# Performance work log

Hardware: AMD Instinct MI355X
Metric: run time of the kernel (lower is better)

Reference implementation:

```python
import jax, jax.numpy as jnp
import numpy as np

B, N, DIM = 2, 2048, 1024
H, DH = 16, 64            # num query heads, head dim (single shared kv head)
CTX_N, CTX_DIM = 256, 1024

def setup_inputs() -> dict:
    key = jax.random.key(0)
    ks = jax.random.split(key, 8)
    s = lambda fan: 1.0 / np.sqrt(fan)
    return {
        'x': jax.random.normal(ks[0], (B, N, DIM), jnp.float32),
        'context': jax.random.normal(ks[1], (B, CTX_N, CTX_DIM), jnp.float32),
        'g1': jnp.ones((DIM,), jnp.float32),
        'Wq': jax.random.normal(ks[2], (DIM, H * DH), jnp.float32) * s(DIM),
        'Wkv': jax.random.normal(ks[3], (DIM, 2 * DH), jnp.float32) * s(DIM),
        'null_kv': jax.random.normal(ks[4], (2, DH), jnp.float32) * s(DH),
        'ctx_g': jnp.ones((CTX_DIM,), jnp.float32),
        'ctx_b': jnp.zeros((CTX_DIM,), jnp.float32),
        'Wc': jax.random.normal(ks[5], (CTX_DIM, 2 * DH), jnp.float32) * s(CTX_DIM),
        'bc': jnp.zeros((2 * DH,), jnp.float32),
        'Wout': jax.random.normal(ks[6], (H * DH, DIM), jnp.float32) * s(H * DH),
        'g2': jnp.ones((DIM,), jnp.float32),
    }

def _ln_g(t, g, eps):
    # custom LayerNorm: scale only, no bias, population variance
    m = jnp.mean(t, axis=-1, keepdims=True)
    v = jnp.var(t, axis=-1, keepdims=True)
    return (t - m) / jnp.sqrt(v + eps) * g

def reference(x, context, g1, Wq, Wkv, null_kv, ctx_g, ctx_b, Wc, bc, Wout, g2):
    b, n, _ = x.shape
    scale = DH ** -0.5
    h = _ln_g(x, g1, 1e-5)                              # [b,n,dim]
    q = (h @ Wq).reshape(b, n, H, DH).transpose(0, 2, 1, 3) * scale  # [b,H,n,d]
    k, v = jnp.split(h @ Wkv, 2, axis=-1)               # each [b,n,d] (single kv head)
    # null kv token
    nk = jnp.broadcast_to(null_kv[0], (b, 1, DH))
    nv = jnp.broadcast_to(null_kv[1], (b, 1, DH))
    k = jnp.concatenate((k, nk), axis=-2)
    v = jnp.concatenate((v, nv), axis=-2)
    # context kv tokens (standard flax LayerNorm: scale+bias, eps=1e-6)
    cm = jnp.mean(context, axis=-1, keepdims=True)
    cv_ = jnp.var(context, axis=-1, keepdims=True)
    ch = (context - cm) / jnp.sqrt(cv_ + 1e-6) * ctx_g + ctx_b
    ck, cvv = jnp.split(ch @ Wc + bc, 2, axis=-1)       # [b,ctx_n,d]
    k = jnp.concatenate((k, ck), axis=-2)               # [b,j,d]
    v = jnp.concatenate((v, cvv), axis=-2)
    sim = jnp.einsum('bhid,bjd->bhij', q, k)            # shared kv head broadcast
    attn = jax.nn.softmax(sim, axis=-1)
    out = jnp.einsum('bhij,bjd->bhid', attn, v)
    out = out.transpose(0, 2, 1, 3).reshape(b, n, H * DH)
    out = out @ Wout
    return _ln_g(out, g2, 1e-5)
```

## Files before the change

### kernel.cpp

```cpp
#include <hip/hip_runtime.h>

typedef __attribute__((ext_vector_type(4)))  float  f32x4;
typedef __attribute__((ext_vector_type(16))) float  f32x16;
typedef __attribute__((ext_vector_type(8)))  short  s16x8;

#define DEVI __device__ __forceinline__

constexpr int Bb   = 2;
constexpr int Nn   = 2048;
constexpr int Hh   = 16;
constexpr int DHc  = 64;
constexpr int CTXN = 256;
constexpr int Jv   = Nn + 1 + CTXN;
constexpr int JP   = 2432;
constexpr int QKVN = Hh*DHc + 2*DHc;

DEVI unsigned short f2bf(float f) {
    union { float f; unsigned u; } v; v.f = f;
    unsigned r = v.u + 0x7fffu + ((v.u >> 16) & 1u);
    return (unsigned short)(r >> 16);
}
DEVI float bf2f(unsigned short h) {
    union { unsigned u; float f; } v; v.u = ((unsigned)h) << 16;
    return v.f;
}
DEVI unsigned cvt_pk_bf(float lo, float hi) {
    unsigned r;
    asm("v_cvt_pk_bf16_f32 %0, %1, %2" : "=v"(r) : "v"(lo), "v"(hi));
    return r;
}
DEVI float exp2v(float x) {
    float r;
    asm("v_exp_f32 %0, %1" : "=v"(r) : "v"(x));
    return r;
}
DEVI void gl_lds16(const void* g, void* l) {
    __builtin_amdgcn_global_load_lds(
        (__attribute__((address_space(1))) void*)g,
        (__attribute__((address_space(3))) void*)l,
        16, 0, 0);
}

__global__ __launch_bounds__(256) void k_pre(const float* __restrict__ Wq,
                                             const float* __restrict__ Wkv,
                                             const float* __restrict__ Wc,
                                             const float* __restrict__ Wout,
                                             const float* __restrict__ x,
                                             const float* __restrict__ ctx,
                                             const float* __restrict__ g1,
                                             const float* __restrict__ cg,
                                             const float* __restrict__ cb,
                                             unsigned short* __restrict__ WqkvT,
                                             unsigned short* __restrict__ WcT,
                                             unsigned short* __restrict__ WoutT,
                                             unsigned short* __restrict__ h,
                                             unsigned short* __restrict__ ch,
                                             float qscale) {
    int bxg = blockIdx.x;
    if (bxg < 2304) {
        __shared__ float tile[32][33];
        int bx = bxg % 72, by = bxg / 72;
        const float* in; unsigned short* out; int C; float scale; int cb_;
        if (bx < 32)      { in = Wq;   out = WqkvT;               C = 1024; scale = qscale; cb_ = bx; }
        else if (bx < 36) { in = Wkv;  out = WqkvT + 1024 * 1024; C = 128;  scale = 1.0f;  cb_ = bx - 32; }
        else if (bx < 40) { in = Wc;   out = WcT;                 C = 128;  scale = 1.0f;  cb_ = bx - 36; }
        else              { in = Wout; out = WoutT;               C = 1024; scale = 1.0f;  cb_ = bx - 40; }
        int tx = threadIdx.x & 31, ty = threadIdx.x >> 5;
        int r0 = by * 32, c0 = cb_ * 32;
#pragma unroll
        for (int i = 0; i < 32; i += 8)
            tile[ty + i][tx] = in[(size_t)(r0 + ty + i) * C + c0 + tx];
        __syncthreads();
#pragma unroll
        for (int i = 0; i < 32; i += 8)
            out[(size_t)(c0 + ty + i) * 1024 + r0 + tx] = f2bf(tile[tx][ty + i] * scale);
    } else {
        int row = bxg - 2304, tid = threadIdx.x;
        bool isx = row < 4096;
        const float* rp = isx ? x + (size_t)row * 1024 : ctx + (size_t)(row - 4096) * 1024;
        const float* g  = isx ? g1 : cg;
        float eps = isx ? 1e-5f : 1e-6f;
        unsigned short* o = isx ? h + (size_t)row * 1024 : ch + (size_t)(row - 4096) * 1024;

        f32x4 v = *(const f32x4*)(rp + tid * 4);
        float s = v.x + v.y + v.z + v.w;
        float q = v.x * v.x + v.y * v.y + v.z * v.z + v.w * v.w;
#pragma unroll
        for (int m = 32; m; m >>= 1) { s += __shfl_down(s, m, 64); q += __shfl_down(q, m, 64); }
        __shared__ float ss[4], sq[4];
        int wid = tid >> 6, lane = tid & 63;
        if (lane == 0) { ss[wid] = s; sq[wid] = q; }
        __syncthreads();
        s = ss[0] + ss[1] + ss[2] + ss[3];
        q = sq[0] + sq[1] + sq[2] + sq[3];
        float mean = s * (1.0f / 1024.0f);
        float var  = q * (1.0f / 1024.0f) - mean * mean;
        float rstd = rsqrtf(var + eps);
        f32x4 gg = *(const f32x4*)(g + tid * 4);
        f32x4 r;
#pragma unroll
        for (int e = 0; e < 4; e++) r[e] = (v[e] - mean) * rstd * gg[e];
        if (!isx) {
            f32x4 bb = *(const f32x4*)(cb + tid * 4);
#pragma unroll
            for (int e = 0; e < 4; e++) r[e] += bb[e];
        }
        uint2 ov = make_uint2(cvt_pk_bf(r[0], r[1]), cvt_pk_bf(r[2], r[3]));
        *(uint2*)(o + tid * 4) = ov;
    }
}

__global__ __launch_bounds__(256) void k_ln_out(const float* __restrict__ in,
                                                const float* __restrict__ g,
                                                float* __restrict__ out) {
    int row = blockIdx.x, tid = threadIdx.x;
    const float* rp = in + (size_t)row * 1024;
    f32x4 v = *(const f32x4*)(rp + tid * 4);
    float s = v.x + v.y + v.z + v.w;
    float q = v.x * v.x + v.y * v.y + v.z * v.z + v.w * v.w;
#pragma unroll
    for (int m = 32; m; m >>= 1) { s += __shfl_down(s, m, 64); q += __shfl_down(q, m, 64); }
    __shared__ float ss[4], sq[4];
    int wid = tid >> 6, lane = tid & 63;
    if (lane == 0) { ss[wid] = s; sq[wid] = q; }
    __syncthreads();
    s = ss[0] + ss[1] + ss[2] + ss[3];
    q = sq[0] + sq[1] + sq[2] + sq[3];
    float mean = s * (1.0f / 1024.0f);
    float var  = q * (1.0f / 1024.0f) - mean * mean;
    float rstd = rsqrtf(var + 1e-5f);
    f32x4 gg = *(const f32x4*)(g + tid * 4);
    f32x4 r;
#pragma unroll
    for (int e = 0; e < 4; e++) r[e] = (v[e] - mean) * rstd * gg[e];
    *(f32x4*)(out + (size_t)row * 1024 + tid * 4) = r;
}

template<int OUT_BF16>
__global__ __launch_bounds__(256) void k_gemm_bt(const unsigned short* __restrict__ A,
                                                 const unsigned short* __restrict__ BT,
                                                 void* __restrict__ C,
                                                 int M, int N, int K) {
    __shared__ unsigned short SA[2][128 * 64];
    __shared__ unsigned short SB[2][64 * 64];
    int tid = threadIdx.x;
    int bn = blockIdx.x, bm = blockIdx.y;
    int wid = tid >> 6, lane = tid & 63;
    int wm = wid >> 1, wn = wid & 1;
    int lr = lane & 15, lg = lane >> 4;
    int r8 = lane >> 3;
    int sl = (lane & 7) ^ r8;

    const unsigned short* Ag = A  + (size_t)(bm * 128 + wid * 32 + r8) * K + sl * 8;
    const unsigned short* Bg = BT + (size_t)(bn * 64  + wid * 16 + r8) * K + sl * 8;

    auto stage = [&](int k0, int buf) {
#pragma unroll
        for (int i = 0; i < 4; i++)
            gl_lds16(Ag + (size_t)i * 8 * K + k0, &SA[buf][wid * 2048 + i * 512]);
#pragma unroll
        for (int i = 0; i < 2; i++)
            gl_lds16(Bg + (size_t)i * 8 * K + k0, &SB[buf][wid * 1024 + i * 512]);
    };

    f32x4 acc[4][2] = {};
    int nk = K >> 6;
    stage(0, 0);
    __syncthreads();
    int cur = 0;
    for (int s = 0; s < nk; ++s) {
        if (s + 1 < nk) stage((s + 1) << 6, cur ^ 1);
        const unsigned short* Al = &SA[cur][0];
        const unsigned short* Bl = &SB[cur][0];
#pragma unroll
        for (int kk = 0; kk < 2; kk++) {
            int co = ((kk * 4 + lg) ^ (lr & 7)) * 8;
            s16x8 af[4], bf[2];
#pragma unroll
            for (int mi = 0; mi < 4; mi++)
                af[mi] = *(const s16x8*)&Al[(wm * 64 + mi * 16 + lr) * 64 + co];
#pragma unroll
            for (int ni = 0; ni < 2; ni++)
                bf[ni] = *(const s16x8*)&Bl[(wn * 32 + ni * 16 + lr) * 64 + co];
#pragma unroll
            for (int mi = 0; mi < 4; mi++)
#pragma unroll
                for (int ni = 0; ni < 2; ni++)
                    acc[mi][ni] = __builtin_amdgcn_mfma_f32_16x16x32_bf16(af[mi], bf[ni], acc[mi][ni], 0, 0, 0);
        }
        __syncthreads();
        cur ^= 1;
    }
#pragma unroll
    for (int mi = 0; mi < 4; mi++)
#pragma unroll
        for (int r = 0; r < 4; r++) {
            int row = bm * 128 + wm * 64 + mi * 16 + lg * 4 + r;
#pragma unroll
            for (int ni = 0; ni < 2; ni++) {
                int col = bn * 64 + wn * 32 + ni * 16 + lr;
                float val = acc[mi][ni][r];
                if (OUT_BF16)
                    ((unsigned short*)C)[(size_t)row * N + col] = f2bf(val);
                else
                    ((float*)C)[(size_t)row * N + col] = val;
            }
        }
}

__global__ __launch_bounds__(256) void k_assemble_kv(const unsigned short* __restrict__ qkv,
                                                     const unsigned short* __restrict__ ckv,
                                                     const float* __restrict__ nkv,
                                                     const float* __restrict__ bc,
                                                     unsigned short* __restrict__ Kb,
                                                     unsigned short* __restrict__ Vt) {
    int idx = blockIdx.x * 256 + threadIdx.x;
    int d = idx & 63;
    int j = (idx >> 6) % JP;
    int b = idx / (64 * JP);
    float kv, vv;
    if (j < Nn) {
        const unsigned short* r = qkv + (size_t)(b * Nn + j) * QKVN + Hh * DHc;
        kv = bf2f(r[d]); vv = bf2f(r[64 + d]);
    } else if (j == Nn) {
        kv = nkv[d]; vv = nkv[64 + d];
    } else if (j < Jv) {
        const unsigned short* r = ckv + (size_t)(b * CTXN + (j - Nn - 1)) * 128;
        kv = bf2f(r[d]) + bc[d]; vv = bf2f(r[64 + d]) + bc[64 + d];
    } else {
        kv = 0.0f; vv = 0.0f;
    }
    Kb[((size_t)b * JP + j) * 64 + d] = f2bf(kv);
    Vt[((size_t)b * 64 + d) * JP + j] = f2bf(vv);
}

__global__ __launch_bounds__(512) void k_attn(const unsigned short* __restrict__ qkv,
                                              const unsigned short* __restrict__ Kb,
                                              const unsigned short* __restrict__ Vt,
                                              unsigned short* __restrict__ aout) {
    __shared__ unsigned short KV[2][2][2][64 * 64];

    int bid = blockIdx.x;
    int qt = bid & 15, h = (bid >> 4) & 15, b = bid >> 8;
    int tid = threadIdx.x, wid = tid >> 6, lane = tid & 63;
    int tm = wid >> 2, tw = wid & 3;
    int l31 = lane & 31, hi = lane >> 5;
    int n0 = qt * 128 + tw * 32;
    int r8 = lane >> 3;
    int sl = (lane & 7) ^ r8;
    int x7 = l31 & 7;
    int jb = tm * 1216;

    s16x8 qf[4];
#pragma unroll
    for (int kk = 0; kk < 4; kk++)
        qf[kk] = *(const s16x8*)(qkv + (size_t)(b * Nn + n0 + l31) * QKVN + h * 64 + kk * 16 + hi * 8);

    f32x16 O0 = {}, O1 = {};
    float Lv = 0.0f;

    const unsigned short* Kg = Kb + ((size_t)b * JP + jb + tw * 16 + r8) * 64 + sl * 8;
    const unsigned short* Vg = Vt + ((size_t)b * 64 + tw * 16 + r8) * JP + jb + sl * 8;

    auto stage = [&](int t, int buf) {
#pragma unroll
        for (int i = 0; i < 2; i++) {
            gl_lds16(Kg + ((size_t)t * 64 + i * 8) * 64, &KV[tm][buf][0][tw * 1024 + i * 512]);
            gl_lds16(Vg + (size_t)i * 8 * JP + t * 64,   &KV[tm][buf][1][tw * 1024 + i * 512]);
        }
    };

    auto build_pf = [&](const f32x16& s, int w) -> s16x8 {
        unsigned c0 = cvt_pk_bf(s[8 * w + 0], s[8 * w + 1]);
        unsigned c1 = cvt_pk_bf(s[8 * w + 2], s[8 * w + 3]);
        unsigned c2 = cvt_pk_bf(s[8 * w + 4], s[8 * w + 5]);
        unsigned c3 = cvt_pk_bf(s[8 * w + 6], s[8 * w + 7]);
        asm("v_permlane32_swap_b32 %0, %1" : "+v"(c0), "+v"(c2));
        asm("v_permlane32_swap_b32 %0, %1" : "+v"(c1), "+v"(c3));
        union { unsigned u[4]; s16x8 v; } pu;
        pu.u[0] = c0; pu.u[1] = c1; pu.u[2] = c2; pu.u[3] = c3;
        return pu.v;
    };

    stage(0, 0);
    __syncthreads();
    int cur = 0;
#pragma unroll 1
    for (int t = 0; t < 19; ++t) {
        if (t < 18) stage(t + 1, cur ^ 1);
        const unsigned short* Kl = &KV[tm][cur][0][0];
        const unsigned short* Vl = &KV[tm][cur][1][0];
        int j0 = jb + t * 64;

        f32x16 s0 = {}, s1 = {};
        __builtin_amdgcn_s_setprio(1);
#pragma unroll
        for (int kk = 0; kk < 4; kk++) {
            int co = ((kk * 2 + hi) ^ x7) * 8;
            s16x8 k0 = *(const s16x8*)&Kl[l31 * 64 + co];
            s16x8 k1 = *(const s16x8*)&Kl[(32 + l31) * 64 + co];
            s0 = __builtin_amdgcn_mfma_f32_32x32x16_bf16(k0, qf[kk], s0, 0, 0, 0);
            s1 = __builtin_amdgcn_mfma_f32_32x32x16_bf16(k1, qf[kk], s1, 0, 0, 0);
        }
        __builtin_amdgcn_s_setprio(0);
        if (j0 + 64 > Jv) {
#pragma unroll
            for (int r = 0; r < 16; r++) {
                int ja = j0 + (r & 3) + 8 * (r >> 2) + 4 * hi;
                if (ja >= Jv)      s0[r] = -1e30f;
                if (ja + 32 >= Jv) s1[r] = -1e30f;
            }
        }

        float sum = 0.0f;
#pragma unroll
        for (int r = 0; r < 16; r++) { s0[r] = exp2v(s0[r]); sum += s0[r]; }
#pragma unroll
        for (int r = 0; r < 16; r++) { s1[r] = exp2v(s1[r]); sum += s1[r]; }
        Lv += sum;

        __builtin_amdgcn_s_setprio(1);
#pragma unroll
        for (int ks = 0; ks < 4; ks++) {
            s16x8 pf = (ks < 2) ? build_pf(s0, ks & 1) : build_pf(s1, ks & 1);
            int co = ((ks * 2 + hi) ^ x7) * 8;
            s16x8 v0 = *(const s16x8*)&Vl[l31 * 64 + co];
            s16x8 v1 = *(const s16x8*)&Vl[(32 + l31) * 64 + co];
            O0 = __builtin_amdgcn_mfma_f32_32x32x16_bf16(v0, pf, O0, 0, 0, 0);
            O1 = __builtin_amdgcn_mfma_f32_32x32x16_bf16(v1, pf, O1, 0, 0, 0);
        }
        __builtin_amdgcn_s_setprio(0);
        __syncthreads();
        cur ^= 1;
    }

    Lv += __shfl_xor(Lv, 32, 64);

    float* Ob = (float*)&KV[0][0][0][0];
    float* Ml = Ob + 4 * 64 * 33;
    unsigned short* slabs = (unsigned short*)(Ml + 4 * 64);

    __syncthreads();
    if (tm == 1) {
        float* dst = Ob + ((size_t)tw * 64 + lane) * 33;
#pragma unroll
        for (int r = 0; r < 16; r++) { dst[r] = O0[r]; dst[16 + r] = O1[r]; }
        Ml[tw * 64 + lane] = Lv;
    }
    __syncthreads();
    if (tm == 0) {
        const float* src = Ob + ((size_t)tw * 64 + lane) * 33;
        float rl = 1.0f / (Lv + Ml[tw * 64 + lane]);

        unsigned short* slab = slabs + tw * 2304;
#pragma unroll
        for (int rq = 0; rq < 4; rq++) {
            uint2 w0 = make_uint2(
                cvt_pk_bf((O0[rq * 4 + 0] + src[rq * 4 + 0]) * rl,
                          (O0[rq * 4 + 1] + src[rq * 4 + 1]) * rl),
                cvt_pk_bf((O0[rq * 4 + 2] + src[rq * 4 + 2]) * rl,
                          (O0[rq * 4 + 3] + src[rq * 4 + 3]) * rl));
            *(uint2*)&slab[l31 * 72 + rq * 8 + hi * 4] = w0;
            uint2 w1 = make_uint2(
                cvt_pk_bf((O1[rq * 4 + 0] + src[16 + rq * 4 + 0]) * rl,
                          (O1[rq * 4 + 1] + src[16 + rq * 4 + 1]) * rl),
                cvt_pk_bf((O1[rq * 4 + 2] + src[16 + rq * 4 + 2]) * rl,
                          (O1[rq * 4 + 3] + src[16 + rq * 4 + 3]) * rl));
            *(uint2*)&slab[l31 * 72 + 32 + rq * 8 + hi * 4] = w1;
        }
        int q = lane >> 1, half = lane & 1;
        const s16x8* srcq = (const s16x8*)&slab[q * 72 + half * 32];
        s16x8 o0 = srcq[0], o1 = srcq[1], o2 = srcq[2], o3 = srcq[3];
        unsigned short* gdst = aout + (size_t)(b * Nn + n0 + q) * 1024 + h * 64 + half * 32;
        *(s16x8*)gdst = o0;
        *((s16x8*)gdst + 1) = o1;
        *((s16x8*)gdst + 2) = o2;
        *((s16x8*)gdst + 3) = o3;
    }
}

extern "C" void kernel_launch(void* const* d_in, const int* in_sizes, int n_in,
                              void* d_out, int out_size, void* d_ws, size_t ws_size,
                              hipStream_t stream) {
    const float* x    = (const float*)d_in[0];
    const float* ctx  = (const float*)d_in[1];
    const float* g1   = (const float*)d_in[2];
    const float* Wq   = (const float*)d_in[3];
    const float* Wkv  = (const float*)d_in[4];
    const float* nkv  = (const float*)d_in[5];
    const float* ctxg = (const float*)d_in[6];
    const float* ctxb = (const float*)d_in[7];
    const float* Wc   = (const float*)d_in[8];
    const float* bc   = (const float*)d_in[9];
    const float* Wout = (const float*)d_in[10];
    const float* g2   = (const float*)d_in[11];
    float* out = (float*)d_out;

    char* w = (char*)d_ws;
    unsigned short* h_    = (unsigned short*)w; w += (size_t)4096 * 1024 * 2;
    unsigned short* ch    = (unsigned short*)w; w += (size_t)512 * 1024 * 2;
    unsigned short* WqkvT = (unsigned short*)w; w += (size_t)1152 * 1024 * 2;
    unsigned short* WcT   = (unsigned short*)w; w += (size_t)128 * 1024 * 2;
    unsigned short* WoutT = (unsigned short*)w; w += (size_t)1024 * 1024 * 2;
    unsigned short* qkv   = (unsigned short*)w; w += (size_t)4096 * 1152 * 2;
    unsigned short* ckv   = (unsigned short*)w; w += (size_t)512 * 128 * 2;
    unsigned short* Kb    = (unsigned short*)w; w += (size_t)Bb * JP * 64 * 2;
    unsigned short* Vt    = (unsigned short*)w; w += (size_t)Bb * 64 * JP * 2;
    unsigned short* aout  = (unsigned short*)w; w += (size_t)4096 * 1024 * 2;
    float* preout         = (float*)w;          w += (size_t)4096 * 1024 * 4;

    const float qscale = 0.125f * 1.4426950408889634f;

    k_pre<<<6912, 256, 0, stream>>>(Wq, Wkv, Wc, Wout, x, ctx, g1, ctxg, ctxb,
                                    WqkvT, WcT, WoutT, h_, ch, qscale);

    k_gemm_bt<1><<<dim3(18, 32), 256, 0, stream>>>(h_, WqkvT, qkv, 4096, 1152, 1024);
    k_gemm_bt<1><<<dim3(2, 4),   256, 0, stream>>>(ch, WcT,   ckv, 512,  128,  1024);

    k_assemble_kv<<<(Bb * JP * 64) / 256, 256, 0, stream>>>(qkv, ckv, nkv, bc, Kb, Vt);

    k_attn<<<Bb * Hh * (Nn / 128), 512, 0, stream>>>(qkv, Kb, Vt, aout);

    k_gemm_bt<0><<<dim3(16, 32), 256, 0, stream>>>(aout, WoutT, preout, 4096, 1024, 1024);
    k_ln_out<<<4096, 256, 0, stream>>>(preout, g2, out);
}
```

Baseline: 121.5 us.

## Triple-buffer GEMM LDS staging and merge QKV and context GEMM launches

The bf16 GEMM moves from double to triple buffering in LDS, prefetching two K-steps ahead. It uses explicit vmcnt waits and raw s_barrier in place of __syncthreads, which keeps more global loads in flight during the MFMA work. The separate QKV and context-KV projection launches are merged into one grid that picks its problem from the block id, removing a launch and letting the small GEMM share the device with the large one. Shared memory per block grows to 72KB, which may lower occupancy, and the hand-counted vmcnt values must match the number of outstanding loads.

```diff
diff --git a/kernel.cpp b/kernel.cpp
--- a/kernel.cpp
+++ b/kernel.cpp
@@ -137,14 +137,12 @@
 }
 
 template<int OUT_BF16>
-__global__ __launch_bounds__(256) void k_gemm_bt(const unsigned short* __restrict__ A,
-                                                 const unsigned short* __restrict__ BT,
-                                                 void* __restrict__ C,
-                                                 int M, int N, int K) {
-    __shared__ unsigned short SA[2][128 * 64];
-    __shared__ unsigned short SB[2][64 * 64];
+DEVI void gemm_core(unsigned short* SAb, unsigned short* SBb,
+                    const unsigned short* __restrict__ A,
+                    const unsigned short* __restrict__ BT,
+                    void* __restrict__ C,
+                    int M, int N, int K, int bn, int bm) {
     int tid = threadIdx.x;
-    int bn = blockIdx.x, bm = blockIdx.y;
     int wid = tid >> 6, lane = tid & 63;
     int wm = wid >> 1, wn = wid & 1;
     int lr = lane & 15, lg = lane >> 4;
@@ -154,24 +152,38 @@
     const unsigned short* Ag = A  + (size_t)(bm * 128 + wid * 32 + r8) * K + sl * 8;
     const unsigned short* Bg = BT + (size_t)(bn * 64  + wid * 16 + r8) * K + sl * 8;
 
-    auto stage = [&](int k0, int buf) {
+    auto stage = [&](int buf, int s) {
+        int k0 = s << 6;
+        unsigned short* SA = SAb + buf * (128 * 64);
+        unsigned short* SB = SBb + buf * (64 * 64);
 #pragma unroll
         for (int i = 0; i < 4; i++)
-            gl_lds16(Ag + (size_t)i * 8 * K + k0, &SA[buf][wid * 2048 + i * 512]);
+            gl_lds16(Ag + (size_t)i * 8 * K + k0, SA + wid * 2048 + i * 512);
 #pragma unroll
         for (int i = 0; i < 2; i++)
-            gl_lds16(Bg + (size_t)i * 8 * K + k0, &SB[buf][wid * 1024 + i * 512]);
+            gl_lds16(Bg + (size_t)i * 8 * K + k0, SB + wid * 1024 + i * 512);
     };
 
     f32x4 acc[4][2] = {};
     int nk = K >> 6;
     stage(0, 0);
-    __syncthreads();
-    int cur = 0;
+    stage(1, 1);
+    int b0 = 0;
+#pragma unroll 1
     for (int s = 0; s < nk; ++s) {
-        if (s + 1 < nk) stage((s + 1) << 6, cur ^ 1);
-        const unsigned short* Al = &SA[cur][0];
-        const unsigned short* Bl = &SB[cur][0];
+        int b2 = b0 + 2; if (b2 >= 3) b2 -= 3;
+        if (s + 2 < nk) {
+            stage(b2, s + 2);
+            asm volatile("s_waitcnt vmcnt(12)" ::: "memory");
+        } else if (s + 1 < nk) {
+            asm volatile("s_waitcnt vmcnt(6)" ::: "memory");
+        } else {
+            asm volatile("s_waitcnt vmcnt(0)" ::: "memory");
+        }
+        __builtin_amdgcn_s_barrier();
+        __builtin_amdgcn_sched_barrier(0);
+        const unsigned short* Al = SAb + b0 * (128 * 64);
+        const unsigned short* Bl = SBb + b0 * (64 * 64);
 #pragma unroll
         for (int kk = 0; kk < 2; kk++) {
             int co = ((kk * 4 + lg) ^ (lr & 7)) * 8;
@@ -188,8 +200,9 @@
                 for (int ni = 0; ni < 2; ni++)
                     acc[mi][ni] = __builtin_amdgcn_mfma_f32_16x16x32_bf16(af[mi], bf[ni], acc[mi][ni], 0, 0, 0);
         }
-        __syncthreads();
-        cur ^= 1;
+        __builtin_amdgcn_sched_barrier(0);
+        __builtin_amdgcn_s_barrier();
+        b0 = b0 + 1; if (b0 >= 3) b0 = 0;
     }
 #pragma unroll
     for (int mi = 0; mi < 4; mi++)
@@ -206,6 +219,32 @@
                     ((float*)C)[(size_t)row * N + col] = val;
             }
         }
+}
+
+__global__ __launch_bounds__(256) void k_gemm_qkv(const unsigned short* __restrict__ h,
+                                                  const unsigned short* __restrict__ WqkvT,
+                                                  unsigned short* __restrict__ qkv,
+                                                  const unsigned short* __restrict__ ch,
+                                                  const unsigned short* __restrict__ WcT,
+                                                  unsigned short* __restrict__ ckv) {
+    __shared__ unsigned short SA[3][128 * 64];
+    __shared__ unsigned short SB[3][64 * 64];
+    int id = blockIdx.x;
+    if (id < 576)
+        gemm_core<1>(&SA[0][0], &SB[0][0], h, WqkvT, qkv, 4096, 1152, 1024, id % 18, id / 18);
+    else {
+        int i2 = id - 576;
+        gemm_core<1>(&SA[0][0], &SB[0][0], ch, WcT, ckv, 512, 128, 1024, i2 % 2, i2 / 2);
+    }
+}
+
+__global__ __launch_bounds__(256) void k_gemm_out(const unsigned short* __restrict__ aout,
+                                                  const unsigned short* __restrict__ WoutT,
+                                                  float* __restrict__ preout) {
+    __shared__ unsigned short SA[3][128 * 64];
+    __shared__ unsigned short SB[3][64 * 64];
+    int id = blockIdx.x;
+    gemm_core<0>(&SA[0][0], &SB[0][0], aout, WoutT, preout, 4096, 1024, 1024, id % 16, id / 16);
 }
 
 __global__ __launch_bounds__(256) void k_assemble_kv(const unsigned short* __restrict__ qkv,
@@ -414,13 +453,12 @@
     k_pre<<<6912, 256, 0, stream>>>(Wq, Wkv, Wc, Wout, x, ctx, g1, ctxg, ctxb,
                                     WqkvT, WcT, WoutT, h_, ch, qscale);
 
-    k_gemm_bt<1><<<dim3(18, 32), 256, 0, stream>>>(h_, WqkvT, qkv, 4096, 1152, 1024);
-    k_gemm_bt<1><<<dim3(2, 4),   256, 0, stream>>>(ch, WcT,   ckv, 512,  128,  1024);
+    k_gemm_qkv<<<584, 256, 0, stream>>>(h_, WqkvT, qkv, ch, WcT, ckv);
 
     k_assemble_kv<<<(Bb * JP * 64) / 256, 256, 0, stream>>>(qkv, ckv, nkv, bc, Kb, Vt);
 
     k_attn<<<Bb * Hh * (Nn / 128), 512, 0, stream>>>(qkv, Kb, Vt, aout);
 
-    k_gemm_bt<0><<<dim3(16, 32), 256, 0, stream>>>(aout, WoutT, preout, 4096, 1024, 1024);
+    k_gemm_out<<<512, 256, 0, stream>>>(aout, WoutT, preout);
     k_ln_out<<<4096, 256, 0, stream>>>(preout, g2, out);
 }
```

Measured after the change: 115.8 us. 1.05x faster.
